# Performance work log

Hardware: AMD Instinct MI355X
Metric: run time of the kernel (lower is better)

## Reference

```python
import jax, jax.numpy as jnp
import numpy as np
import math

N_HEADS = 16
D_MODEL = 1024
M = D_MODEL // N_HEADS  # per-head dim = 64

def _kaiming_uniform(key, shape):
    # torch kaiming_uniform_ with a=sqrt(5) on [h, fan_in, fan_out]-style 3D tensor:
    # fan_in = shape[1] (size of dim 1), gain = sqrt(2/(1+a^2)) = sqrt(1/3)
    fan_in = shape[1]
    gain = math.sqrt(2.0 / (1.0 + 5.0))
    bound = gain * math.sqrt(3.0 / fan_in)
    return jax.random.uniform(key, shape, dtype=jnp.float32, minval=-bound, maxval=bound)

def setup_inputs() -> dict:
    key = jax.random.key(0)
    kx, kq, kk, kv, ko = jax.random.split(key, 5)
    x = jax.random.normal(kx, (4, 2048, D_MODEL), dtype=jnp.float32)
    W_q = _kaiming_uniform(kq, (N_HEADS, D_MODEL, M))
    W_k = _kaiming_uniform(kk, (N_HEADS, D_MODEL, M))
    W_v = _kaiming_uniform(kv, (N_HEADS, D_MODEL, M))
    W_o = _kaiming_uniform(ko, (N_HEADS, M, D_MODEL))
    return {"x": x, "W_q": W_q, "W_k": W_k, "W_v": W_v, "W_o": W_o}

def reference(x, W_q, W_k, W_v, W_o):
    # x: [b, s, d]; W_q/W_k/W_v: [h, d, m]; W_o: [h, m, d]
    q = jnp.einsum('bsd,hdm->bhsm', x, W_q)
    k = jnp.einsum('bsd,hdm->bhsm', x, W_k)
    v = jnp.einsum('bsd,hdm->bhsm', x, W_v)
    scale = 1.0 / math.sqrt(q.shape[-1])
    scores = jnp.einsum('bhsm,bhtm->bhst', q, k) * scale  # [b,h,s,s]
    attn = jax.nn.softmax(scores, axis=-1)
    ctx = jnp.einsum('bhst,bhtm->bhsm', attn, v)
    out = jnp.einsum('bhsm,hmd->bsd', ctx, W_o)  # sum over heads
    return out
```

## Files before the change

### kernel.cpp

```cpp
#include <hip/hip_runtime.h>
#include <hip/hip_bf16.h>

typedef __attribute__((ext_vector_type(8))) short short8;
typedef __attribute__((ext_vector_type(8))) _Float16 half8;
typedef __attribute__((ext_vector_type(4))) float f32x4;
typedef __attribute__((ext_vector_type(16))) float f32x16;
typedef __attribute__((ext_vector_type(4))) unsigned int uint4v;

#define NB 4
#define NH 16
#define NS 2048
#define ND 1024
#define NM 64
#define R_TOT 8192
#define N_QKV 3072
#define QKV_ONE 8388608
#define SCALE_Q 0.18033688011112042f

static __device__ __forceinline__ unsigned short f2h(float f) {
    _Float16 h = (_Float16)f;
    return __builtin_bit_cast(unsigned short, h);
}
static __device__ __forceinline__ unsigned cvtpk_h(float lo, float hiv) {
    unsigned r;
    asm("v_cvt_pkrtz_f16_f32 %0, %1, %2" : "=v"(r) : "v"(lo), "v"(hiv));
    return r;
}
static __device__ __forceinline__ void gl_lds16(const unsigned short* g, unsigned short* l) {
    __builtin_amdgcn_global_load_lds((const __attribute__((address_space(1))) void*)g,
                                     (__attribute__((address_space(3))) void*)l, 16, 0, 0);
}
static __device__ __forceinline__ half8 rd_swz(const unsigned short* base, int row, int col) {
    int byte = (row << 7) + (col << 1);
    byte ^= (row & 7) << 4;
    return *(const half8*)((const char*)base + byte);
}

__global__ __launch_bounds__(256) void k_convert_x(const float* __restrict__ x,
                                                   unsigned short* __restrict__ xh) {
    int i = blockIdx.x * 256 + threadIdx.x;
    const float4* xp = (const float4*)x;
    float4 v = xp[i];
    ushort4 o;
    o.x = f2h(v.x); o.y = f2h(v.y); o.z = f2h(v.z); o.w = f2h(v.w);
    ((ushort4*)xh)[i] = o;
}

__global__ __launch_bounds__(256) void k_convert_wqkv(const float* __restrict__ Wq,
                                                      const float* __restrict__ Wk,
                                                      const float* __restrict__ Wv,
                                                      unsigned short* __restrict__ BT) {
    int i = blockIdx.x * 256 + threadIdx.x;
    int d = i & 1023;
    int n = i >> 10;
    int w = n >> 10;
    int h = (n >> 6) & 15;
    int m = n & 63;
    const float* W = (w == 0) ? Wq : ((w == 1) ? Wk : Wv);
    float v = W[((size_t)h * ND + d) * NM + m];
    if (w == 0) v *= SCALE_Q;
    BT[i] = f2h(v);
}

__global__ __launch_bounds__(256) void k_convert_wo(const float* __restrict__ Wo,
                                                    unsigned short* __restrict__ BTo) {
    int i = blockIdx.x * 256 + threadIdx.x;
    int n = i & 1023;
    int d = i >> 10;
    BTo[i] = f2h(Wo[(size_t)n * ND + d]);
}

__global__ __launch_bounds__(256) void k_gemm_qkv(const unsigned short* __restrict__ A,
                                                  const unsigned short* __restrict__ BT,
                                                  unsigned short* __restrict__ qkv) {
    __shared__ unsigned short As[128 * 64];
    __shared__ unsigned short Bs[128 * 64];
    int tid = threadIdx.x;
    int bx = blockIdx.x;
    int rt = bx & 63;
    int ct = bx >> 6;
    int r0 = rt * 128, c0 = ct * 128;
    int lane = tid & 63, wid = tid >> 6;
    int l15 = lane & 15, grp = lane >> 4;
    int wr = (wid >> 1) * 64, wc = (wid & 1) * 64;

    f32x4 acc[4][4] = {};

    for (int k0 = 0; k0 < 1024; k0 += 64) {
        #pragma unroll
        for (int i = 0; i < 4; ++i) {
            int seg = wid * 4 + i;
            int row = seg * 8 + (lane >> 3);
            int sch = (lane & 7) ^ (row & 7);
            gl_lds16(A + (size_t)(r0 + row) * 1024 + k0 + sch * 8, As + seg * 512 + lane * 8);
            gl_lds16(BT + (size_t)(c0 + row) * 1024 + k0 + sch * 8, Bs + seg * 512 + lane * 8);
        }
        __syncthreads();
        #pragma unroll
        for (int ks = 0; ks < 64; ks += 32) {
            half8 af[4], bf[4];
            #pragma unroll
            for (int i = 0; i < 4; ++i)
                af[i] = rd_swz(As, wr + i * 16 + l15, ks + grp * 8);
            #pragma unroll
            for (int j = 0; j < 4; ++j)
                bf[j] = rd_swz(Bs, wc + j * 16 + l15, ks + grp * 8);
            #pragma unroll
            for (int i = 0; i < 4; ++i)
                #pragma unroll
                for (int j = 0; j < 4; ++j)
                    acc[i][j] = __builtin_amdgcn_mfma_f32_16x16x32_f16(af[i], bf[j], acc[i][j], 0, 0, 0);
        }
        __syncthreads();
    }
    #pragma unroll
    for (int j = 0; j < 4; ++j) {
        int n_base = c0 + wc + j * 16;
        int w = n_base >> 10;
        int nh = n_base + l15;
        int h = (nh >> 6) & 15;
        int m = nh & 63;
        if (w == 2) {
            unsigned short* outp = qkv + 2 * (size_t)QKV_ONE;
            #pragma unroll
            for (int i = 0; i < 4; ++i) {
                int rb = r0 + wr + i * 16 + grp * 4;
                int bb = rb >> 11, s = rb & 2047;
                ushort4 pv;
                pv.x = f2h(acc[i][j][0]);
                pv.y = f2h(acc[i][j][1]);
                pv.z = f2h(acc[i][j][2]);
                pv.w = f2h(acc[i][j][3]);
                *(ushort4*)(outp + ((size_t)(bb * NH + h) * NM + m) * NS + s) = pv;
            }
        } else {
            unsigned short* outp = qkv + (size_t)w * QKV_ONE;
            #pragma unroll
            for (int i = 0; i < 4; ++i) {
                int rb = r0 + wr + i * 16 + grp * 4;
                #pragma unroll
                for (int reg = 0; reg < 4; ++reg) {
                    int r = rb + reg;
                    int bb = r >> 11, s = r & 2047;
                    outp[((size_t)(bb * NH + h) * NS + s) * NM + m] = f2h(acc[i][j][reg]);
                }
            }
        }
    }
}

__global__ __launch_bounds__(512) void k_attn(const unsigned short* __restrict__ qkv,
                                              unsigned short* __restrict__ ctx) {
    __shared__ unsigned short Ks[2][4096];
    __shared__ unsigned short Vs[2][4096];

    int tid = threadIdx.x;
    int lane = tid & 63, wid = tid >> 6;
    int l31 = lane & 31, hi = lane >> 5;

    int bid = blockIdx.x;
    int xcd = bid & 7;
    int j = bid >> 3;
    int bh = xcd * 8 + (j >> 3);
    int qb = j & 7;
    int b = bh >> 4, h = bh & 15;

    size_t hb = (size_t)bh * NS * NM;
    const unsigned short* Qg = qkv + hb;
    const unsigned short* Kg = qkv + QKV_ONE + hb;
    const unsigned short* Vt = qkv + 2 * (size_t)QKV_ONE + hb;

    int q0 = qb * 256 + wid * 32;

    half8 qf[4];
    #pragma unroll
    for (int kk = 0; kk < 4; ++kk)
        qf[kk] = *(const half8*)(Qg + (size_t)(q0 + l31) * NM + kk * 16 + hi * 8);

    half8 ones;
    #pragma unroll
    for (int e = 0; e < 8; ++e) ones[e] = (_Float16)1.0f;

    f32x16 accO0 = {}, accO1 = {}, accS = {};

    const unsigned short* gsrc0;
    const unsigned short* gsrc1;
    unsigned short* lbase0;
    unsigned short* lbase1;
    int step0, step1;
    {
        int seg = wid * 2;
        int off = (seg & 7) * 512 + lane * 8;
        int row = off >> 6;
        int sch = ((off >> 3) & 7) ^ (row & 7);
        if (seg < 8) { gsrc0 = Kg + row * NM + sch * 8; step0 = NM;  lbase0 = &Ks[0][off]; }
        else         { gsrc0 = Vt + (size_t)row * NS + sch * 8; step0 = 1; lbase0 = &Vs[0][off]; }
        seg = wid * 2 + 1;
        off = (seg & 7) * 512 + lane * 8;
        row = off >> 6;
        sch = ((off >> 3) & 7) ^ (row & 7);
        if (seg < 8) { gsrc1 = Kg + row * NM + sch * 8; step1 = NM;  lbase1 = &Ks[0][off]; }
        else         { gsrc1 = Vt + (size_t)row * NS + sch * 8; step1 = 1; lbase1 = &Vs[0][off]; }
    }
    auto stage = [&](int bufi, int t0) {
        gl_lds16(gsrc0 + (size_t)t0 * step0, lbase0 + bufi * 4096);
        gl_lds16(gsrc1 + (size_t)t0 * step1, lbase1 + bufi * 4096);
    };

    stage(0, 0);
    stage(1, 64);

    for (int t = 0; t < 32; ++t) {
        int buf = t & 1;
        if (t < 31) asm volatile("s_waitcnt vmcnt(2)" ::: "memory");
        else        asm volatile("s_waitcnt vmcnt(0)" ::: "memory");
        __builtin_amdgcn_s_barrier();
        __builtin_amdgcn_sched_barrier(0);
        const unsigned short* Kb = Ks[buf];
        const unsigned short* Vb = Vs[buf];

        f32x16 s0v = {}, s1v = {};
        __builtin_amdgcn_s_setprio(1);
        #pragma unroll
        for (int kk = 0; kk < 4; ++kk) {
            int col = kk * 16 + hi * 8;
            s0v = __builtin_amdgcn_mfma_f32_32x32x16_f16(rd_swz(Kb, l31, col), qf[kk], s0v, 0, 0, 0);
            s1v = __builtin_amdgcn_mfma_f32_32x32x16_f16(rd_swz(Kb, 32 + l31, col), qf[kk], s1v, 0, 0, 0);
        }
        __builtin_amdgcn_s_setprio(0);

        unsigned pk0[8], pk1[8];
        #pragma unroll
        for (int jj = 0; jj < 8; ++jj) {
            float a0 = __builtin_amdgcn_exp2f(s0v[2 * jj]);
            float b0 = __builtin_amdgcn_exp2f(s0v[2 * jj + 1]);
            float a1 = __builtin_amdgcn_exp2f(s1v[2 * jj]);
            float b1 = __builtin_amdgcn_exp2f(s1v[2 * jj + 1]);
            pk0[jj] = cvtpk_h(a0, b0);
            pk1[jj] = cvtpk_h(a1, b1);
        }

        __builtin_amdgcn_s_setprio(1);
        #pragma unroll
        for (int kt = 0; kt < 4; ++kt) {
            unsigned w0, w1, w2, w3;
            if (kt < 2) {
                int base = (kt & 1) * 4;
                w0 = pk0[base + 0]; w1 = pk0[base + 1];
                w2 = pk0[base + 2]; w3 = pk0[base + 3];
            } else {
                int base = (kt & 1) * 4;
                w0 = pk1[base + 0]; w1 = pk1[base + 1];
                w2 = pk1[base + 2]; w3 = pk1[base + 3];
            }
            asm("v_permlane32_swap_b32 %0, %1" : "+v"(w0), "+v"(w2));
            asm("v_permlane32_swap_b32 %0, %1" : "+v"(w1), "+v"(w3));
            uint4v av;
            av[0] = w0; av[1] = w1; av[2] = w2; av[3] = w3;
            half8 af = __builtin_bit_cast(half8, av);
            int col = kt * 16 + hi * 8;
            accO0 = __builtin_amdgcn_mfma_f32_32x32x16_f16(af, rd_swz(Vb, l31, col), accO0, 0, 0, 0);
            accO1 = __builtin_amdgcn_mfma_f32_32x32x16_f16(af, rd_swz(Vb, 32 + l31, col), accO1, 0, 0, 0);
            accS  = __builtin_amdgcn_mfma_f32_32x32x16_f16(af, ones, accS, 0, 0, 0);
        }
        __builtin_amdgcn_s_setprio(0);

        __builtin_amdgcn_sched_barrier(0);
        __builtin_amdgcn_s_barrier();
        if (t < 30) stage(buf, (t + 2) * 64);
    }

    #pragma unroll
    for (int reg = 0; reg < 16; ++reg) {
        int q = (reg & 3) + 8 * (reg >> 2) + 4 * hi;
        float linv = 1.0f / accS[reg];
        size_t ob = ((size_t)b * NS + (q0 + q)) * ND + h * 64 + l31;
        ctx[ob] = f2h(accO0[reg] * linv);
        ctx[ob + 32] = f2h(accO1[reg] * linv);
    }
}

__global__ __launch_bounds__(256) void k_gemm_out(const unsigned short* __restrict__ A,
                                                  const unsigned short* __restrict__ BT,
                                                  float* __restrict__ Cf) {
    __shared__ unsigned short As[128 * 64];
    __shared__ unsigned short Bs[128 * 64];
    int tid = threadIdx.x;
    int bx = blockIdx.x;
    int rt = bx & 63, ct = bx >> 6;
    int r0 = rt * 128, c0 = ct * 128;
    int lane = tid & 63, wid = tid >> 6;
    int l15 = lane & 15, grp = lane >> 4;
    int wr = (wid >> 1) * 64, wc = (wid & 1) * 64;
    f32x4 acc[4][4] = {};

    for (int k0 = 0; k0 < 1024; k0 += 64) {
        #pragma unroll
        for (int i = 0; i < 4; ++i) {
            int seg = wid * 4 + i;
            int row = seg * 8 + (lane >> 3);
            int sch = (lane & 7) ^ (row & 7);
            gl_lds16(A + (size_t)(r0 + row) * 1024 + k0 + sch * 8, As + seg * 512 + lane * 8);
            gl_lds16(BT + (size_t)(c0 + row) * 1024 + k0 + sch * 8, Bs + seg * 512 + lane * 8);
        }
        __syncthreads();
        #pragma unroll
        for (int ks = 0; ks < 64; ks += 32) {
            half8 af[4], bf[4];
            #pragma unroll
            for (int i = 0; i < 4; ++i)
                af[i] = rd_swz(As, wr + i * 16 + l15, ks + grp * 8);
            #pragma unroll
            for (int j = 0; j < 4; ++j)
                bf[j] = rd_swz(Bs, wc + j * 16 + l15, ks + grp * 8);
            #pragma unroll
            for (int i = 0; i < 4; ++i)
                #pragma unroll
                for (int j = 0; j < 4; ++j)
                    acc[i][j] = __builtin_amdgcn_mfma_f32_16x16x32_f16(af[i], bf[j], acc[i][j], 0, 0, 0);
        }
        __syncthreads();
    }
    #pragma unroll
    for (int i = 0; i < 4; ++i)
        #pragma unroll
        for (int j = 0; j < 4; ++j)
            #pragma unroll
            for (int reg = 0; reg < 4; ++reg) {
                int r = r0 + wr + i * 16 + grp * 4 + reg;
                int c = c0 + wc + j * 16 + l15;
                Cf[(size_t)r * 1024 + c] = acc[i][j][reg];
            }
}

extern "C" void kernel_launch(void* const* d_in, const int* in_sizes, int n_in,
                              void* d_out, int out_size, void* d_ws, size_t ws_size,
                              hipStream_t stream) {
    (void)in_sizes; (void)n_in; (void)out_size; (void)ws_size;
    const float* x  = (const float*)d_in[0];
    const float* Wq = (const float*)d_in[1];
    const float* Wk = (const float*)d_in[2];
    const float* Wv = (const float*)d_in[3];
    const float* Wo = (const float*)d_in[4];

    char* ws = (char*)d_ws;
    unsigned short* Xh   = (unsigned short*)ws;  ws += (size_t)R_TOT * 1024 * 2;
    unsigned short* BTq  = (unsigned short*)ws;  ws += (size_t)N_QKV * 1024 * 2;
    unsigned short* BTo  = (unsigned short*)ws;  ws += (size_t)1024 * 1024 * 2;
    unsigned short* QKV  = (unsigned short*)ws;  ws += (size_t)3 * QKV_ONE * 2;
    unsigned short* Ctx  = (unsigned short*)ws;  ws += (size_t)R_TOT * 1024 * 2;

    k_convert_x<<<dim3(R_TOT * 1024 / 4 / 256), dim3(256), 0, stream>>>(x, Xh);
    k_convert_wqkv<<<dim3(N_QKV * 1024 / 256), dim3(256), 0, stream>>>(Wq, Wk, Wv, BTq);
    k_convert_wo<<<dim3(1024 * 1024 / 256), dim3(256), 0, stream>>>(Wo, BTo);
    k_gemm_qkv<<<dim3(64 * 24), dim3(256), 0, stream>>>(Xh, BTq, QKV);
    k_attn<<<dim3(512), dim3(512), 0, stream>>>(QKV, Ctx);
    k_gemm_out<<<dim3(64 * 8), dim3(256), 0, stream>>>(Ctx, BTo, (float*)d_out);
}
```

Measured before the change: 198.6 us.

## Restructure QKV GEMM into larger double-buffered tiles with block swizzle

The QKV projection GEMM moves from 128x128 tiles with 256 threads and a sync-bound single buffer to 256x192 tiles with 512 threads, double-buffered LDS, and prefetch of the next K-slice issued while MFMAs run. A block-index swizzle groups tiles for better L2 reuse, and setprio wraps the MFMA bursts. The intent is to hide global-load latency and cut barrier stalls and redundant traffic, at the cost of much more LDS and register pressure. In the attention kernel, inline asm for the permlane32 swap is replaced by the compiler builtin.

New measurement: 193.0 us, median of 2. 2.8% less time.

```diff
diff --git a/kernel.cpp b/kernel.cpp
--- a/kernel.cpp
+++ b/kernel.cpp
@@ -6,6 +6,7 @@
 typedef __attribute__((ext_vector_type(4))) float f32x4;
 typedef __attribute__((ext_vector_type(16))) float f32x16;
 typedef __attribute__((ext_vector_type(4))) unsigned int uint4v;
+typedef __attribute__((ext_vector_type(2))) unsigned int uint2v;
 
 #define NB 4
 #define NH 16
@@ -70,52 +71,88 @@
     BTo[i] = f2h(Wo[(size_t)n * ND + d]);
 }
 
-__global__ __launch_bounds__(256) void k_gemm_qkv(const unsigned short* __restrict__ A,
-                                                  const unsigned short* __restrict__ BT,
-                                                  unsigned short* __restrict__ qkv) {
-    __shared__ unsigned short As[128 * 64];
-    __shared__ unsigned short Bs[128 * 64];
+#define QBM 256
+#define QBN 192
+__global__ __launch_bounds__(512, 2) void k_gemm_qkv(const unsigned short* __restrict__ A,
+                                                     const unsigned short* __restrict__ BT,
+                                                     unsigned short* __restrict__ qkv) {
+    __shared__ unsigned short L[2][(QBM + QBN) * 64];
     int tid = threadIdx.x;
     int bx = blockIdx.x;
-    int rt = bx & 63;
-    int ct = bx >> 6;
-    int r0 = rt * 128, c0 = ct * 128;
+    int swz = (bx & 7) * 64 + (bx >> 3);
+    int rt = swz & 31;
+    int ct = swz >> 5;
+    int r0 = rt * QBM, c0 = ct * QBN;
     int lane = tid & 63, wid = tid >> 6;
     int l15 = lane & 15, grp = lane >> 4;
-    int wr = (wid >> 1) * 64, wc = (wid & 1) * 64;
-
-    f32x4 acc[4][4] = {};
-
-    for (int k0 = 0; k0 < 1024; k0 += 64) {
-        #pragma unroll
-        for (int i = 0; i < 4; ++i) {
-            int seg = wid * 4 + i;
-            int row = seg * 8 + (lane >> 3);
-            int sch = (lane & 7) ^ (row & 7);
-            gl_lds16(A + (size_t)(r0 + row) * 1024 + k0 + sch * 8, As + seg * 512 + lane * 8);
-            gl_lds16(BT + (size_t)(c0 + row) * 1024 + k0 + sch * 8, Bs + seg * 512 + lane * 8);
-        }
-        __syncthreads();
-        #pragma unroll
-        for (int ks = 0; ks < 64; ks += 32) {
-            half8 af[4], bf[4];
-            #pragma unroll
-            for (int i = 0; i < 4; ++i)
-                af[i] = rd_swz(As, wr + i * 16 + l15, ks + grp * 8);
-            #pragma unroll
-            for (int j = 0; j < 4; ++j)
-                bf[j] = rd_swz(Bs, wc + j * 16 + l15, ks + grp * 8);
-            #pragma unroll
-            for (int i = 0; i < 4; ++i)
-                #pragma unroll
-                for (int j = 0; j < 4; ++j)
-                    acc[i][j] = __builtin_amdgcn_mfma_f32_16x16x32_f16(af[i], bf[j], acc[i][j], 0, 0, 0);
-        }
-        __syncthreads();
-    }
-    #pragma unroll
-    for (int j = 0; j < 4; ++j) {
-        int n_base = c0 + wc + j * 16;
+    int wrow = (wid >> 2) * 128;
+    int wcol = (wid & 3) * 48;
+
+    f32x4 acc[8][3] = {};
+
+    auto stageA = [&](int bufi, int k0) {
+        #pragma unroll
+        for (int r = 0; r < 4; ++r) {
+            int off = r * 4096 + tid * 8;
+            int row = off >> 6;
+            int sch = ((off >> 3) & 7) ^ (row & 7);
+            gl_lds16(A + (size_t)(r0 + row) * 1024 + k0 + sch * 8, &L[bufi][off]);
+        }
+    };
+    auto stageB = [&](int bufi, int k0) {
+        #pragma unroll
+        for (int r = 0; r < 3; ++r) {
+            int off = r * 4096 + tid * 8;
+            int row = off >> 6;
+            int sch = ((off >> 3) & 7) ^ (row & 7);
+            gl_lds16(BT + (size_t)(c0 + row) * 1024 + k0 + sch * 8, &L[bufi][QBM * 64 + off]);
+        }
+    };
+
+    stageA(0, 0);
+    stageB(0, 0);
+    asm volatile("s_waitcnt vmcnt(0)" ::: "memory");
+    __builtin_amdgcn_s_barrier();
+
+    for (int t = 0; t < 16; ++t) {
+        int buf = t & 1;
+        const unsigned short* As = L[buf];
+        const unsigned short* Bs = L[buf] + QBM * 64;
+
+        half8 af[8], bf[3];
+        #pragma unroll
+        for (int i = 0; i < 8; ++i) af[i] = rd_swz(As, wrow + i * 16 + l15, grp * 8);
+        #pragma unroll
+        for (int j = 0; j < 3; ++j) bf[j] = rd_swz(Bs, wcol + j * 16 + l15, grp * 8);
+        if (t < 15) { stageA(buf ^ 1, (t + 1) * 64); stageB(buf ^ 1, (t + 1) * 64); }
+        __builtin_amdgcn_sched_barrier(0);
+        __builtin_amdgcn_s_setprio(1);
+        #pragma unroll
+        for (int i = 0; i < 8; ++i)
+            #pragma unroll
+            for (int j = 0; j < 3; ++j)
+                acc[i][j] = __builtin_amdgcn_mfma_f32_16x16x32_f16(af[i], bf[j], acc[i][j], 0, 0, 0);
+        __builtin_amdgcn_s_setprio(0);
+
+        #pragma unroll
+        for (int i = 0; i < 8; ++i) af[i] = rd_swz(As, wrow + i * 16 + l15, 32 + grp * 8);
+        #pragma unroll
+        for (int j = 0; j < 3; ++j) bf[j] = rd_swz(Bs, wcol + j * 16 + l15, 32 + grp * 8);
+        __builtin_amdgcn_s_setprio(1);
+        #pragma unroll
+        for (int i = 0; i < 8; ++i)
+            #pragma unroll
+            for (int j = 0; j < 3; ++j)
+                acc[i][j] = __builtin_amdgcn_mfma_f32_16x16x32_f16(af[i], bf[j], acc[i][j], 0, 0, 0);
+        __builtin_amdgcn_s_setprio(0);
+
+        asm volatile("s_waitcnt vmcnt(0)" ::: "memory");
+        __builtin_amdgcn_s_barrier();
+    }
+
+    #pragma unroll
+    for (int j = 0; j < 3; ++j) {
+        int n_base = c0 + wcol + j * 16;
         int w = n_base >> 10;
         int nh = n_base + l15;
         int h = (nh >> 6) & 15;
@@ -123,8 +160,8 @@
         if (w == 2) {
             unsigned short* outp = qkv + 2 * (size_t)QKV_ONE;
             #pragma unroll
-            for (int i = 0; i < 4; ++i) {
-                int rb = r0 + wr + i * 16 + grp * 4;
+            for (int i = 0; i < 8; ++i) {
+                int rb = r0 + wrow + i * 16 + grp * 4;
                 int bb = rb >> 11, s = rb & 2047;
                 ushort4 pv;
                 pv.x = f2h(acc[i][j][0]);
@@ -136,8 +173,8 @@
         } else {
             unsigned short* outp = qkv + (size_t)w * QKV_ONE;
             #pragma unroll
-            for (int i = 0; i < 4; ++i) {
-                int rb = r0 + wr + i * 16 + grp * 4;
+            for (int i = 0; i < 8; ++i) {
+                int rb = r0 + wrow + i * 16 + grp * 4;
                 #pragma unroll
                 for (int reg = 0; reg < 4; ++reg) {
                     int r = rb + reg;
@@ -253,10 +290,10 @@
                 w0 = pk1[base + 0]; w1 = pk1[base + 1];
                 w2 = pk1[base + 2]; w3 = pk1[base + 3];
             }
-            asm("v_permlane32_swap_b32 %0, %1" : "+v"(w0), "+v"(w2));
-            asm("v_permlane32_swap_b32 %0, %1" : "+v"(w1), "+v"(w3));
+            uint2v r02 = __builtin_amdgcn_permlane32_swap(w0, w2, false, false);
+            uint2v r13 = __builtin_amdgcn_permlane32_swap(w1, w3, false, false);
             uint4v av;
-            av[0] = w0; av[1] = w1; av[2] = w2; av[3] = w3;
+            av[0] = r02[0]; av[1] = r13[0]; av[2] = r02[1]; av[3] = r13[1];
             half8 af = __builtin_bit_cast(half8, av);
             int col = kt * 16 + hi * 8;
             accO0 = __builtin_amdgcn_mfma_f32_32x32x16_f16(af, rd_swz(Vb, l31, col), accO0, 0, 0, 0);
@@ -353,7 +390,7 @@
     k_convert_x<<<dim3(R_TOT * 1024 / 4 / 256), dim3(256), 0, stream>>>(x, Xh);
     k_convert_wqkv<<<dim3(N_QKV * 1024 / 256), dim3(256), 0, stream>>>(Wq, Wk, Wv, BTq);
     k_convert_wo<<<dim3(1024 * 1024 / 256), dim3(256), 0, stream>>>(Wo, BTo);
-    k_gemm_qkv<<<dim3(64 * 24), dim3(256), 0, stream>>>(Xh, BTq, QKV);
+    k_gemm_qkv<<<dim3(512), dim3(512), 0, stream>>>(Xh, BTq, QKV);
     k_attn<<<dim3(512), dim3(512), 0, stream>>>(QKV, Ctx);
     k_gemm_out<<<dim3(64 * 8), dim3(256), 0, stream>>>(Ctx, BTo, (float*)d_out);
 }
```
